# Kernel optimization log

Hardware: AMD Instinct MI355X
Metric: run time of the kernel (lower is better)

## Reference

```python
import jax, jax.numpy as jnp
import numpy as np

D = 1024   # hidden_size
H = 16     # n_head
K = 64     # head_size
B = 4
T = 1024
LAYER_ID = 12
NUM_LAYERS = 24
D_MIX = 32
D_DECAY = 64


def setup_inputs() -> dict:
    key = jax.random.key(0)
    ks = jax.random.split(key, 12)
    r01 = LAYER_ID / (NUM_LAYERS - 1)          # ratio_0_to_1
    r10 = 1.0 - LAYER_ID / NUM_LAYERS          # ratio_1_to_almost0
    ddd = jnp.arange(D, dtype=jnp.float32) / D
    maa = lambda p: (1.0 - ddd ** p).reshape(1, 1, D)
    inp = {}
    inp['x'] = jax.random.normal(ks[0], (B, T, D), jnp.float32)
    inp['time_maa_x'] = maa(r10)
    inp['time_maa_w'] = maa(r10)
    inp['time_maa_k'] = maa(r10)
    inp['time_maa_v'] = (1.0 - (ddd ** r10 + 0.3 * r01)).reshape(1, 1, D)
    inp['time_maa_r'] = maa(0.5 * r10)
    inp['time_maa_g'] = maa(0.5 * r10)
    # torch inits time_maa_w1 to zeros (trivial); use small uniform like w2 for a non-degenerate test
    inp['time_maa_w1'] = jax.random.uniform(ks[1], (D, D_MIX * 5), jnp.float32, -0.01, 0.01)
    inp['time_maa_w2'] = jax.random.uniform(ks[2], (5, D_MIX, D), jnp.float32, -0.01, 0.01)
    n = jnp.arange(D, dtype=jnp.float32)
    inp['time_decay'] = (-6.0 + 5.0 * (n / (D - 1)) ** (0.7 + 1.3 * r01)).reshape(1, 1, D)
    inp['time_decay_w1'] = jax.random.uniform(ks[3], (D, D_DECAY), jnp.float32, -0.01, 0.01)
    inp['time_decay_w2'] = jax.random.uniform(ks[4], (D_DECAY, D), jnp.float32, -0.01, 0.01)
    for nm, kk in zip(['W_r', 'W_k', 'W_v', 'W_g', 'W_o'], ks[5:10]):
        inp[nm] = jax.random.normal(kk, (D, D), jnp.float32) * 0.02
    inp['ln_w'] = jnp.ones((D,), jnp.float32)
    inp['ln_b'] = jnp.zeros((D,), jnp.float32)
    return inp


def _bidir_shift(x):
    # (x[i-1] + x[i+1]) / 2 with zero padding at the boundaries
    left = jnp.pad(x[:, :-1, :], ((0, 0), (1, 0), (0, 0)))
    right = jnp.pad(x[:, 1:, :], ((0, 0), (0, 1), (0, 0)))
    return 0.5 * (left + right)


def _lion_attention(r, k, v, w):
    # r,k,v,w: (B,H,T,Khd), w = -exp(decay) <= 0
    Tn = r.shape[2]
    cs = jnp.cumsum(w, axis=2)
    cs_b = cs - w
    shift_f = cs[:, :, Tn // 2:Tn // 2 + 1, :]
    shift_b = cs_b[:, :, Tn // 2:Tn // 2 + 1, :]
    cf = jnp.clip(cs - shift_f, -60.0, 60.0)
    cb = jnp.clip(cs_b - shift_b, -60.0, 60.0)
    # A_fwd = tril(Q*e^{cf} @ (K*e^{-cf})^T); A_bwd = triu(Q*e^{-cb} @ (K*e^{cb})^T, 1)
    A_f = jnp.einsum('bhik,bhjk->bhij', r * jnp.exp(cf), k * jnp.exp(-cf))
    A_b = jnp.einsum('bhik,bhjk->bhij', r * jnp.exp(-cb), k * jnp.exp(cb))
    idx = jnp.arange(Tn)
    lower = idx[:, None] >= idx[None, :]   # tril incl. diagonal
    A = jnp.where(lower, A_f, A_b)         # == tril(A_f) + triu(A_b, 1)
    return jnp.einsum('bhij,bhjk->bhik', A, v)


def reference(x, time_maa_x, time_maa_w, time_maa_k, time_maa_v, time_maa_r, time_maa_g,
              time_maa_w1, time_maa_w2, time_decay, time_decay_w1, time_decay_w2,
              W_r, W_k, W_v, W_g, W_o, ln_w, ln_b):
    Bn, Tn, Dn = x.shape
    Hh, Kk = H, Dn // H
    dxprev = _bidir_shift(x) - x
    # data-dependent token-shift mixing coefficients (LoRA-style)
    xxx = jnp.tanh((x + dxprev * time_maa_x) @ time_maa_w1)          # (B,T,5*32)
    mm = jnp.einsum('btfm,fmd->fbtd', xxx.reshape(Bn, Tn, 5, D_MIX), time_maa_w2)
    mw, mk, mv, mr, mg = mm[0], mm[1], mm[2], mm[3], mm[4]
    xw = x + dxprev * (time_maa_w + mw)
    xk = x + dxprev * (time_maa_k + mk)
    xv = x + dxprev * (time_maa_v + mv)
    xr = x + dxprev * (time_maa_r + mr)
    xg = x + dxprev * (time_maa_g + mg)
    r = xr @ W_r.T
    k = xk @ W_k.T
    v = xv @ W_v.T
    g = jax.nn.silu(xg @ W_g.T)
    w = time_decay + jnp.tanh(xw @ time_decay_w1) @ time_decay_w2   # (B,T,D)
    to_h = lambda t: t.reshape(Bn, Tn, Hh, Kk).transpose(0, 2, 1, 3)
    y = _lion_attention(to_h(r), to_h(k), to_h(v), -jnp.exp(to_h(w)))
    y = y.transpose(0, 2, 1, 3).reshape(Bn * Tn, Dn)
    # GroupNorm(n_head groups, eps = 1e-5 * head_size_divisor^2)
    eps = 1e-5 * 64.0
    yg = y.reshape(Bn * Tn, Hh, Kk)
    mu = jnp.mean(yg, axis=-1, keepdims=True)
    var = jnp.var(yg, axis=-1, keepdims=True)
    yn = ((yg - mu) * jax.lax.rsqrt(var + eps)).reshape(Bn * Tn, Dn) * ln_w + ln_b
    y = yn.reshape(Bn, Tn, Dn)
    return (y * g) @ W_o.T
```

## Files before the change

kernel.cpp:

```cpp
#include <hip/hip_runtime.h>
#include <math.h>

#define NB 4
#define TT 1024
#define DD 1024
#define NTOK 4096
#define ND (NTOK*DD)

typedef __attribute__((ext_vector_type(8))) short bh8;
typedef __attribute__((ext_vector_type(4))) float fx4;

__device__ __forceinline__ unsigned short f2bf(float f) {
    unsigned int b = __float_as_uint(f);
    b += 0x7fffu + ((b >> 16) & 1u);
    return (unsigned short)(b >> 16);
}

__device__ __forceinline__ unsigned pkbf(float a, float b) {
#if __has_builtin(__builtin_amdgcn_cvt_pk_bf16_f32)
    auto r = __builtin_amdgcn_cvt_pk_bf16_f32(a, b);
    unsigned u;
    __builtin_memcpy(&u, &r, 4);
    return u;
#else
// ... 21 lines not shown
    if (y < 5) {
        if (bx >= 512) return;
        const float* s = (y == 0) ? W_r : (y == 1) ? W_k : (y == 2) ? W_v : (y == 3) ? W_g : W_o;
        unsigned short* d = (y == 0) ? Wrb : (y == 1) ? Wkb : (y == 2) ? Wvb : (y == 3) ? Wgb : Wob;
        int i = (bx * 256 + tid) * 8;
        float4 a = *(const float4*)(s + i);
        float4 b = *(const float4*)(s + i + 4);
        uint4 o;
        o.x = pkbf(a.x, a.y);
        o.y = pkbf(a.z, a.w);
        o.z = pkbf(b.x, b.y);
        o.w = pkbf(b.z, b.w);
        *(uint4*)(d + i) = o;
    } else if (y == 5) {
        int o = bx * 256 + tid;
        int r = o & 1023, c = o >> 10;
        w1T[o] = f2bf(w1[r * 160 + c]);
    } else {
        if (bx < 256) {
            int o = bx * 256 + tid;
            int r = o & 1023, c = o >> 10;
            dw1T[o] = f2bf(dw1[r * 64 + c]);
        } else if (bx < 276) {
            int wi = bx - 256;
            int f = wi >> 2;
            int d = (wi & 3) * 256 + tid;
#pragma unroll 8
            for (int m = 0; m < 32; m++)
                w2T16[(size_t)(f * 1024 + d) * 32 + m] = f2bf(w2[(size_t)(f * 32 + m) * 1024 + d]);
        }
    }
}

__global__ __launch_bounds__(256) void k_mixx(const float* __restrict__ x,
                                              const float* __restrict__ maa_x,
                                              unsigned short* __restrict__ xmix16) {
    int base = (blockIdx.x * 256 + threadIdx.x) * 4;
    int t = (base >> 10) & 1023;
    int d = base & 1023;
    float4 xv = *(const float4*)(x + base);
    float4 xm = (t > 0)    ? *(const float4*)(x + base - 1024) : make_float4(0, 0, 0, 0);
    float4 xp = (t < 1023) ? *(const float4*)(x + base + 1024) : make_float4(0, 0, 0, 0);
    float4 ma = *(const float4*)(maa_x + d);
    uint2 o;
    float a0 = xv.x + (0.5f * (xm.x + xp.x) - xv.x) * ma.x;
    float a1 = xv.y + (0.5f * (xm.y + xp.y) - xv.y) * ma.y;
    float a2 = xv.z + (0.5f * (xm.z + xp.z) - xv.z) * ma.z;
    float a3 = xv.w + (0.5f * (xm.w + xp.w) - xv.w) * ma.w;
    o.x = pkbf(a0, a1);
    o.y = pkbf(a2, a3);
    *(uint2*)(xmix16 + base) = o;
}

__global__ __launch_bounds__(64) void k_xxx2(const unsigned short* __restrict__ xmix16,
                                             const unsigned short* __restrict__ w1T,
                                             unsigned short* __restrict__ xxx16) {
    int lane = threadIdx.x;
    int l15 = lane & 15, qd = lane >> 4;
    int m0 = blockIdx.x * 16;
    fx4 acc[10];
#pragma unroll
    for (int nt = 0; nt < 10; nt++)
#pragma unroll
        for (int r = 0; r < 4; r++) acc[nt][r] = 0.f;
#pragma unroll 2
    for (int kb = 0; kb < 1024; kb += 32) {
        bh8 af = *(const bh8*)(xmix16 + (size_t)(m0 + l15) * 1024 + kb + qd * 8);
#pragma unroll
        for (int nt = 0; nt < 10; nt++) {
            bh8 bf = *(const bh8*)(w1T + (size_t)(nt * 16 + l15) * 1024 + kb + qd * 8);
            acc[nt] = __builtin_amdgcn_mfma_f32_16x16x32_bf16(af, bf, acc[nt], 0, 0, 0);
        }
    }
#pragma unroll
    for (int nt = 0; nt < 10; nt++)
#pragma unroll
        for (int r = 0; r < 4; r++)
            xxx16[(size_t)(m0 + qd * 4 + r) * 160 + nt * 16 + l15] = f2bf(tanhf(acc[nt][r]));
}

__global__ __launch_bounds__(256, 2) void k_mmix(const float* __restrict__ x,
                                                 const unsigned short* __restrict__ xxx16,
                                                 const unsigned short* __restrict__ w2T16,
                                                 const float* __restrict__ maa_w,
                                                 const float* __restrict__ maa_k,
                                                 const float* __restrict__ maa_v,
                                                 const float* __restrict__ maa_r,
                                                 const float* __restrict__ maa_g,
                                                 unsigned short* __restrict__ xw16,
                                                 unsigned short* __restrict__ xk16,
                                                 unsigned short* __restrict__ xv16,
                                                 unsigned short* __restrict__ xr16,
                                                 unsigned short* __restrict__ xg16) {
    int tid = threadIdx.x;
    int w = tid >> 6, lane = tid & 63, l15 = lane & 15, qd = lane >> 4;
    int n0 = blockIdx.x * 64;
    int m0w = blockIdx.y * 128 + w * 32;
    const float* maap[5] = {maa_w, maa_k, maa_v, maa_r, maa_g};
    unsigned short* outp[5] = {xw16, xk16, xv16, xr16, xg16};
    float xin[8][4], dxv[8][4];
#pragma unroll
    for (int mi = 0; mi < 2; mi++)
#pragma unroll
        for (int r = 0; r < 4; r++) {
            int tok = m0w + mi * 16 + qd * 4 + r;
            int t = tok & 1023;
#pragma unroll
            for (int ni = 0; ni < 4; ni++) {
                int d = n0 + ni * 16 + l15;
                size_t idx = (size_t)tok * 1024 + d;
                float xv = x[idx];
                float xm1 = (t > 0)    ? x[idx - 1024] : 0.f;
                float xp1 = (t < 1023) ? x[idx + 1024] : 0.f;
                xin[mi * 4 + r][ni] = xv;
                dxv[mi * 4 + r][ni] = 0.5f * (xm1 + xp1) - xv;
            }
        }
#pragma unroll
    for (int f = 0; f < 5; f++) {
        bh8 af[2], bf[4];
#pragma unroll
        for (int mi = 0; mi < 2; mi++)
            af[mi] = *(const bh8*)(xxx16 + (size_t)(m0w + mi * 16 + l15) * 160 + f * 32 + qd * 8);
#pragma unroll
        for (int ni = 0; ni < 4; ni++)
            bf[ni] = *(const bh8*)(w2T16 + (size_t)(f * 1024 + n0 + ni * 16 + l15) * 32 + qd * 8);
        fx4 acc[2][4];
#pragma unroll
        for (int mi = 0; mi < 2; mi++)
#pragma unroll
            for (int ni = 0; ni < 4; ni++) {
#pragma unroll
                for (int r = 0; r < 4; r++) acc[mi][ni][r] = 0.f;
                acc[mi][ni] = __builtin_amdgcn_mfma_f32_16x16x32_bf16(af[mi], bf[ni], acc[mi][ni], 0, 0, 0);
            }
        const float* maa = maap[f];
        unsigned short* op = outp[f];
#pragma unroll
        for (int ni = 0; ni < 4; ni++) {
            float mv = maa[n0 + ni * 16 + l15];
#pragma unroll
            for (int mi = 0; mi < 2; mi++)
#pragma unroll
                for (int r = 0; r < 4; r++) {
                    float o = xin[mi * 4 + r][ni] + dxv[mi * 4 + r][ni] * (mv + acc[mi][ni][r]);
                    op[(size_t)(m0w + mi * 16 + qd * 4 + r) * 1024 + n0 + ni * 16 + l15] = f2bf(o);
                }
        }
    }
}

__global__ __launch_bounds__(64) void k_dec1m(const unsigned short* __restrict__ xw16,
                                              const unsigned short* __restrict__ dw1T,
                                              float* __restrict__ dech) {
    int lane = threadIdx.x;
    int l15 = lane & 15, qd = lane >> 4;
    int m0 = blockIdx.x * 16;
    fx4 acc[4];
#pragma unroll
    for (int nt = 0; nt < 4; nt++)
#pragma unroll
        for (int r = 0; r < 4; r++) acc[nt][r] = 0.f;
#pragma unroll 2
    for (int kb = 0; kb < 1024; kb += 32) {
        bh8 af = *(const bh8*)(xw16 + (size_t)(m0 + l15) * 1024 + kb + qd * 8);
#pragma unroll
        for (int nt = 0; nt < 4; nt++) {
            bh8 bf = *(const bh8*)(dw1T + (size_t)(nt * 16 + l15) * 1024 + kb + qd * 8);
            acc[nt] = __builtin_amdgcn_mfma_f32_16x16x32_bf16(af, bf, acc[nt], 0, 0, 0);
        }
    }
#pragma unroll
    for (int nt = 0; nt < 4; nt++)
#pragma unroll
        for (int r = 0; r < 4; r++)
            dech[(size_t)(m0 + qd * 4 + r) * 64 + nt * 16 + l15] = tanhf(acc[nt][r]);
}

__global__ __launch_bounds__(256) void k_dec2(const float* __restrict__ dech,
                                              const float* __restrict__ dw2,
                                              const float* __restrict__ tdec,
                                              float* __restrict__ ew) {
    __shared__ float hl[8][64];
    int tid = threadIdx.x;
    int tok0 = blockIdx.x * 8;
    {
        int l = tid;        hl[l >> 6][l & 63] = dech[tok0 * 64 + l];
        l = tid + 256;      hl[l >> 6][l & 63] = dech[tok0 * 64 + l];
    }
    __syncthreads();
#pragma unroll 1
    for (int c = 0; c < 4; c++) {
        int d = c * 256 + tid;
        float acc[8] = {};
#pragma unroll 8
        for (int j = 0; j < 64; j++) {
            float wv = dw2[j * 1024 + d];
#pragma unroll
            for (int g = 0; g < 8; g++) acc[g] = fmaf(hl[g][j], wv, acc[g]);
        }
        float td = tdec[d];
#pragma unroll
        for (int g = 0; g < 8; g++) ew[(tok0 + g) * 1024 + d] = -expf(td + acc[g]);
    }
}

__global__ __launch_bounds__(64) void k_scan1(const float* __restrict__ ew, float* __restrict__ segsum) {
    int bx = blockIdx.x;
    int b = bx >> 9, seg = (bx >> 4) & 31, dch = bx & 15;
    int d = dch * 64 + threadIdx.x;
    size_t base = ((size_t)(b * 1024 + seg * 32)) * 1024 + d;
    float s = 0.f;
#pragma unroll 8
    for (int t = 0; t < 32; t++) s += ew[base + (size_t)t * 1024];
    segsum[(b * 32 + seg) * 1024 + d] = s;
}

__global__ __launch_bounds__(64) void k_scan3(const float* __restrict__ ew, const float* __restrict__ segsum,
                                              float* __restrict__ cf, float* __restrict__ cb) {
    int bx = blockIdx.x;
    int b = bx >> 9, seg = (bx >> 4) & 31, dch = bx & 15;
    int d = dch * 64 + threadIdx.x;
    float run = 0.f, pre = 0.f, off16 = 0.f;
#pragma unroll
    for (int s = 0; s < 32; s++) {
        float tv = segsum[(b * 32 + s) * 1024 + d];
        if (s == seg) pre = run;
        if (s == 16) off16 = run;
        run += tv;
    }
    float e512 = ew[((size_t)(b * 1024 + 512)) * 1024 + d];
    float sb = off16;
    float sf = off16 + e512;
    float cum = pre;
    size_t base = ((size_t)(b * 1024 + seg * 32)) * 1024 + d;
#pragma unroll 4
    for (int t = 0; t < 32; t++) {
        float prev = cum;
        cum += ew[base + (size_t)t * 1024];
        cf[base + (size_t)t * 1024] = fminf(fmaxf(cum - sf, -60.f), 60.f);
        cb[base + (size_t)t * 1024] = fminf(fmaxf(prev - sb, -60.f), 60.f);
    }
}

__device__ __forceinline__ void gemm_body(const unsigned short* __restrict__ A,
                                          const unsigned short* __restrict__ W,
                                          int m0, int n0, int mode,
                                          float* __restrict__ Cf,
                                          unsigned short* __restrict__ O1,
                                          unsigned short* __restrict__ O2,
                                          const float* __restrict__ cfp,
                                          const float* __restrict__ cbp,
                                          char* smem) {
    int tid = threadIdx.x;
    int w = tid >> 6, lane = tid & 63, l15 = lane & 15, qd = lane >> 4;
    int wm = w >> 1, wn = w & 1;
    fx4 acc[4][4];
#pragma unroll
    for (int mt = 0; mt < 4; mt++)
#pragma unroll
        for (int nt = 0; nt < 4; nt++)
#pragma unroll
            for (int r = 0; r < 4; r++) acc[mt][nt][r] = 0.f;
    unsigned short* sA = (unsigned short*)smem;
    unsigned short* sB = (unsigned short*)(smem + 8192);
    int rowA = tid >> 2, cA = tid & 3;
    for (int kb = 0; kb < 1024; kb += 32) {
        __syncthreads();
        GLD16(A + (size_t)(m0 + rowA) * 1024 + kb + cA * 8,      sA + w * 512);
        GLD16(A + (size_t)(m0 + 64 + rowA) * 1024 + kb + cA * 8, sA + 2048 + w * 512);
        GLD16(W + (size_t)(n0 + rowA) * 1024 + kb + cA * 8,      sB + w * 512);
        GLD16(W + (size_t)(n0 + 64 + rowA) * 1024 + kb + cA * 8, sB + 2048 + w * 512);
        __syncthreads();
        bh8 af[4], bfr[4];
#pragma unroll
        for (int mt = 0; mt < 4; mt++)
            af[mt] = *(const bh8*)(sA + (wm * 64 + mt * 16 + l15) * 32 + qd * 8);
#pragma unroll
        for (int nt = 0; nt < 4; nt++)
            bfr[nt] = *(const bh8*)(sB + (wn * 64 + nt * 16 + l15) * 32 + qd * 8);
#pragma unroll
        for (int mt = 0; mt < 4; mt++)
#pragma unroll
            for (int nt = 0; nt < 4; nt++)
                acc[mt][nt] = __builtin_amdgcn_mfma_f32_16x16x32_bf16(af[mt], bfr[nt], acc[mt][nt], 0, 0, 0);
    }
    int mb = m0 + wm * 64, nb = n0 + wn * 64;
    if (mode <= 1) {
#pragma unroll
        for (int mt = 0; mt < 4; mt++)
#pragma unroll
            for (int nt = 0; nt < 4; nt++) {
                fx4 s = acc[mt][nt];
#pragma unroll
                for (int r = 0; r < 4; r++) {
                    float v = s[r];
                    if (mode == 1) v = v / (1.f + __expf(-v));
                    Cf[(size_t)(mb + mt * 16 + qd * 4 + r) * 1024 + nb + nt * 16 + l15] = v;
                }
            }
    } else if (mode <= 3) {
        float s1 = (mode == 2) ? 1.f : -1.f;
#pragma unroll
        for (int mt = 0; mt < 4; mt++)
#pragma unroll
            for (int nt = 0; nt < 4; nt++) {
                fx4 s = acc[mt][nt];
#pragma unroll
                for (int r = 0; r < 4; r++) {
                    size_t idx = (size_t)(mb + mt * 16 + qd * 4 + r) * 1024 + nb + nt * 16 + l15;
                    float v = s[r];
                    O1[idx] = f2bf(v * __expf(s1 * cfp[idx]));
                    O2[idx] = f2bf(v * __expf(-s1 * cbp[idx]));
                }
            }
    } else {
        __syncthreads();
        unsigned short* T = (unsigned short*)smem;
#pragma unroll
        for (int mt = 0; mt < 4; mt++)
#pragma unroll
            for (int nt = 0; nt < 4; nt++) {
                fx4 s = acc[mt][nt];
                int dl = wn * 64 + nt * 16 + l15;
                int tl = wm * 64 + mt * 16 + qd * 4;
                uint2 pk;
                pk.x = pkbf(s[0], s[1]);
                pk.y = pkbf(s[2], s[3]);
                *(uint2*)(T + dl * 136 + tl) = pk;
            }
        __syncthreads();
        int dl = tid >> 1, hf = tid & 1;
        int bq = m0 >> 10, t0 = m0 & 1023;
#pragma unroll
        for (int i = 0; i < 8; i++) {
            uint4 vv4 = *(const uint4*)(T + dl * 136 + hf * 64 + i * 8);
            *(uint4*)(O1 + (size_t)(bq * 1024 + n0 + dl) * 1024 + t0 + hf * 64 + i * 8) = vv4;
        }
    }
}


#define STA(dstbuf, g, kbv, Apt) GLD16(Apt + (size_t)(m0 + aBase + (g) * 32 + lr) * 1024 + (kbv) + swz, \
                                       (dstbuf) + (aBase + (g) * 32) * 64)
#define STB(dstbuf, s, kbv, Wpt) GLD16(Wpt + (size_t)(n0 + bBase + (s) * 64 + lr) * 1024 + (kbv) + swz, \
                                       (dstbuf) + (bBase + (s) * 64) * 64)

#define PHASE(mt0_, STAGE_, TAIL_) do {                                                  \
    bh8 aA0 = *(const bh8*)(sAc + arA + (mt0_) * 1024 + fc0);                            \
    bh8 aA1 = *(const bh8*)(sAc + arA + (mt0_) * 1024 + fc1);                            \
    bh8 aB0 = *(const bh8*)(sAc + arA + ((mt0_) + 1) * 1024 + fc0);                      \
    bh8 aB1 = *(const bh8*)(sAc + arA + ((mt0_) + 1) * 1024 + fc1);                      \
    STAGE_;                                                                              \
    BARF();                                                                              \
    asm volatile("s_waitcnt lgkmcnt(0)" ::: "memory");                                   \
    __builtin_amdgcn_s_setprio(1);                                                       \
    _Pragma("unroll")                                                                    \
    for (int nt = 0; nt < 4; ++nt) {                                                     \
        acc[(mt0_)][nt]     = __builtin_amdgcn_mfma_f32_16x16x32_bf16(aA0, bfr[nt][0], acc[(mt0_)][nt], 0, 0, 0);     \
        acc[(mt0_)][nt]     = __builtin_amdgcn_mfma_f32_16x16x32_bf16(aA1, bfr[nt][1], acc[(mt0_)][nt], 0, 0, 0);     \
        acc[(mt0_) + 1][nt] = __builtin_amdgcn_mfma_f32_16x16x32_bf16(aB0, bfr[nt][0], acc[(mt0_) + 1][nt], 0, 0, 0); \
        acc[(mt0_) + 1][nt] = __builtin_amdgcn_mfma_f32_16x16x32_bf16(aB1, bfr[nt][1], acc[(mt0_) + 1][nt], 0, 0, 0); \
    }                                                                                    \
    __builtin_amdgcn_s_setprio(0);                                                       \
    TAIL_;                                                                               \
    BARF();                                                                              \
} while (0)

__global__ __launch_bounds__(512, 2) void k_qkvg(const unsigned short* __restrict__ xr16,
                                                 const unsigned short* __restrict__ xk16,
                                                 const unsigned short* __restrict__ xv16,
                                                 const unsigned short* __restrict__ xg16,
                                                 const unsigned short* __restrict__ Wrb,
                                                 const unsigned short* __restrict__ Wkb,
                                                 const unsigned short* __restrict__ Wvb,
                                                 const unsigned short* __restrict__ Wgb,
                                                 unsigned short* __restrict__ qf, unsigned short* __restrict__ qb,
                                                 unsigned short* __restrict__ kf, unsigned short* __restrict__ kb,
                                                 unsigned short* __restrict__ vvt,
                                                 float* __restrict__ gg,
                                                 const float* __restrict__ cf, const float* __restrict__ cb) {
    __shared__ __align__(16) char smem[131072];
    unsigned short* sA0 = (unsigned short*)smem;
    unsigned short* sB0 = (unsigned short*)(smem + 32768);
    unsigned short* sA1 = (unsigned short*)(smem + 65536);
    unsigned short* sB1 = (unsigned short*)(smem + 98304);

    int flat = blockIdx.x;
    int wk = (flat & 7) * 32 + (flat >> 3);
    int gy = wk >> 6;
    int wi = wk & 63;
    int m0 = (wi >> 2) * 256, n0 = (wi & 3) * 256;

    const unsigned short* Ap = (gy == 0) ? xr16 : (gy == 1) ? xk16 : (gy == 2) ? xv16 : xg16;
// ... 66 lines not shown
#pragma unroll
                for (int r = 0; r < 4; r++) {
                    float v = acc[mt][nt][r];
                    v = v / (1.f + __expf(-v));
                    gg[(size_t)(mb + mt * 16 + qd * 4 + r) * 1024 + nb + nt * 16 + l15] = v;
                }
    } else if (gy == 2) {
        __syncthreads();
        unsigned short* T = (unsigned short*)smem;
        int bq = m0 >> 10, t0 = m0 & 1023;
#pragma unroll 1
        for (int h = 0; h < 2; ++h) {
            if (wm == h) {
#pragma unroll
                for (int mt = 0; mt < 8; mt++)
#pragma unroll
                    for (int nt = 0; nt < 4; nt++) {
                        int dl = wn * 64 + nt * 16 + l15;
                        int rl = mt * 16 + qd * 4;
                        uint2 pk;
                        pk.x = pkbf(acc[mt][nt][0], acc[mt][nt][1]);
                        pk.y = pkbf(acc[mt][nt][2], acc[mt][nt][3]);
                        *(uint2*)(T + dl * 136 + rl) = pk;
                    }
            }
            __syncthreads();
#pragma unroll
            for (int i = 0; i < 8; ++i) {
                int gch = i * 512 + tid;
                int d = gch >> 4, tch = gch & 15;
                uint4 vv = *(const uint4*)(T + d * 136 + tch * 8);
                *(uint4*)(vvt + (size_t)(bq * 1024 + n0 + d) * 1024 + t0 + h * 128 + tch * 8) = vv;
            }
            __syncthreads();
        }
    } else {
        unsigned short* O1 = gy ? kf : qf;
        unsigned short* O2 = gy ? kb : qb;
        float s1 = gy ? -1.f : 1.f;
#pragma unroll
        for (int mt = 0; mt < 8; mt++)
#pragma unroll
            for (int nt = 0; nt < 4; nt++)
#pragma unroll
                for (int r = 0; r < 4; r++) {
                    size_t idx = (size_t)(mb + mt * 16 + qd * 4 + r) * 1024 + nb + nt * 16 + l15;
                    float v = acc[mt][nt][r];
                    O1[idx] = f2bf(v * __expf(s1 * cf[idx]));
                    O2[idx] = f2bf(v * __expf(-s1 * cb[idx]));
                }
    }
}

__global__ __launch_bounds__(256, 2) void k_gemmo(const unsigned short* __restrict__ z16,
                                                  const unsigned short* __restrict__ Wob,
                                                  float* __restrict__ out) {
    __shared__ __align__(16) char smem[34816];
    gemm_body(z16, Wob, (blockIdx.x >> 3) * 128, (blockIdx.x & 7) * 128, 0, out,
              nullptr, nullptr, nullptr, nullptr, smem);
}

__global__ __launch_bounds__(256, 2) void k_attn(const unsigned short* __restrict__ qf,
                                                 const unsigned short* __restrict__ qb,
                                                 const unsigned short* __restrict__ kf,
                                                 const unsigned short* __restrict__ kb,
                                                 const unsigned short* __restrict__ vvt,
                                                 float* __restrict__ y) {
    __shared__ __align__(16) char smem[16384];
    unsigned short* sK = (unsigned short*)smem;
    unsigned short* sV = (unsigned short*)(smem + 8192);
    int tid = threadIdx.x;
    int w = tid >> 6, lane = tid & 63, l15 = lane & 15, qd = lane >> 4;
    int bid = blockIdx.x;
    int bh = (bid & 7) + ((bid >> 6) << 3);
    int ib = (bid >> 3) & 7;
    int b = bh >> 4, h = bh & 15;
    int i0w = ib * 128 + w * 32;
    int bt0 = b * 1024;
    const unsigned short* vrow = vvt + (size_t)(b * 1024 + h * 64 + w * 16 + l15) * 1024 + qd * 8;
    int fmax = (i0w + 31) >> 6;
    int bmin = i0w >> 6;
    int srcA = l15 + ((lane & 16) << 1);
    int srcB = srcA + 16;
    fx4 yacc[4][2];
#pragma unroll
    for (int mt = 0; mt < 4; mt++)
#pragma unroll
        for (int nt = 0; nt < 2; nt++)
#pragma unroll
            for (int r = 0; r < 4; r++) yacc[mt][nt][r] = 0.f;

    for (int phase = 0; phase < 2; phase++) {
        const unsigned short* Q = phase ? qb : qf;
        const unsigned short* K = phase ? kb : kf;
        bh8 qfr[2][2];
#pragma unroll
        for (int nt = 0; nt < 2; nt++)
#pragma unroll
            for (int ks = 0; ks < 2; ks++)
                qfr[nt][ks] = *(const bh8*)(Q + (size_t)(bt0 + i0w + nt * 16 + l15) * 1024
                                              + h * 64 + ks * 32 + qd * 8);
        int jlo = phase == 0 ? 0 : 2 * ib;
        int jhi = phase == 0 ? 2 * ib + 1 : 15;
        const unsigned short* krow = K + (size_t)(bt0 + w * 16 + l15) * 1024 + h * 64 + qd * 8;
        for (int jt = jlo; jt <= jhi; jt++) {
            int jb = jt * 64;
            __syncthreads();
            GLD16(krow + (size_t)jb * 1024,        sK + w * 512);
            GLD16(krow + (size_t)jb * 1024 + 32,   sK + 2048 + w * 512);
            GLD16(vrow + jb,                        sV + w * 512);
            GLD16(vrow + jb + 32,                   sV + 2048 + w * 512);
            __syncthreads();
            bool active = (phase == 0) ? (jt <= fmax) : (jt >= bmin);
            if (!active) continue;
            bool needmask = (phase == 0) ? (jb + 63 > i0w) : (i0w + 31 >= jb);
            bh8 kc[8];
#pragma unroll
            for (int fi = 0; fi < 8; fi++)
                kc[fi] = *(const bh8*)(sK + fi * 512 + lane * 8);
            fx4 sacc[4][2];
#pragma unroll
            for (int mt = 0; mt < 4; mt++)
#pragma unroll
                for (int nt = 0; nt < 2; nt++)
#pragma unroll
                    for (int r = 0; r < 4; r++) sacc[mt][nt][r] = 0.f;
#pragma unroll
            for (int ks = 0; ks < 2; ks++)
#pragma unroll
                for (int mt = 0; mt < 4; mt++)
#pragma unroll
                    for (int nt = 0; nt < 2; nt++)
                        sacc[mt][nt] = __builtin_amdgcn_mfma_f32_16x16x32_bf16(kc[ks * 4 + mt], qfr[nt][ks], sacc[mt][nt], 0, 0, 0);
            uint2 pk[4][2];
#pragma unroll
            for (int mt = 0; mt < 4; mt++)
#pragma unroll
                for (int nt = 0; nt < 2; nt++) {
                    fx4 s = sacc[mt][nt];
                    if (needmask) {
                        int ii = i0w + nt * 16 + l15;
                        int jj0 = jb + mt * 16 + qd * 4;
#pragma unroll
                        for (int r = 0; r < 4; r++) {
                            bool keep = (phase == 0) ? (ii >= jj0 + r) : (ii < jj0 + r);
                            if (!keep) s[r] = 0.f;
                        }
                    }
                    pk[mt][nt].x = pkbf(s[0], s[1]);
                    pk[mt][nt].y = pkbf(s[2], s[3]);
                }
            bh8 vc[8];
#pragma unroll
            for (int fi = 0; fi < 8; fi++)
                vc[fi] = *(const bh8*)(sV + fi * 512 + lane * 8);
#pragma unroll
            for (int ks2 = 0; ks2 < 2; ks2++) {
#pragma unroll
                for (int nt = 0; nt < 2; nt++) {
                    int lox  = __shfl((int)pk[2 * ks2][nt].x,     srcA);
                    int hix  = __shfl((int)pk[2 * ks2 + 1][nt].x, srcA);
                    int loy  = __shfl((int)pk[2 * ks2][nt].y,     srcA);
                    int hiy  = __shfl((int)pk[2 * ks2 + 1][nt].y, srcA);
                    int lox2 = __shfl((int)pk[2 * ks2][nt].x,     srcB);
                    int hix2 = __shfl((int)pk[2 * ks2 + 1][nt].x, srcB);
                    int loy2 = __shfl((int)pk[2 * ks2][nt].y,     srcB);
                    int hiy2 = __shfl((int)pk[2 * ks2 + 1][nt].y, srcB);
                    union { int4 i; bh8 h; } cv;
                    cv.i.x = (qd & 2) ? hix  : lox;
                    cv.i.y = (qd & 2) ? hiy  : loy;
                    cv.i.z = (qd & 2) ? hix2 : lox2;
                    cv.i.w = (qd & 2) ? hiy2 : loy2;
#pragma unroll
                    for (int mt = 0; mt < 4; mt++)
                        yacc[mt][nt] = __builtin_amdgcn_mfma_f32_16x16x32_bf16(vc[ks2 * 4 + mt], cv.h, yacc[mt][nt], 0, 0, 0);
                }
            }
        }
    }
#pragma unroll
    for (int mt = 0; mt < 4; mt++)
#pragma unroll
        for (int nt = 0; nt < 2; nt++) {
            fx4 s = yacc[mt][nt];
            float4 o; o.x = s[0]; o.y = s[1]; o.z = s[2]; o.w = s[3];
            *(float4*)&y[(size_t)(bt0 + i0w + nt * 16 + l15) * 1024 + h * 64 + mt * 16 + qd * 4] = o;
        }
}

__global__ __launch_bounds__(256) void k_gn(const float* __restrict__ y,
                                            const float* __restrict__ g,
                                            const float* __restrict__ lnw,
                                            const float* __restrict__ lnb,
                                            unsigned short* __restrict__ z16) {
    int tid = threadIdx.x;
    int lane = tid & 63;
    int wv = tid >> 6;
    int group = blockIdx.x * 4 + wv;
    int tok = group >> 4, h = group & 15;
    int d = h * 64 + lane;
    size_t idx = (size_t)tok * 1024 + d;
    float val = y[idx];
    float s = val, s2 = val * val;
#pragma unroll
    for (int off = 32; off > 0; off >>= 1) {
        s  += __shfl_xor(s, off, 64);
        s2 += __shfl_xor(s2, off, 64);
    }
    float mu = s * (1.f / 64.f);
    float var = s2 * (1.f / 64.f) - mu * mu;
    float inv = rsqrtf(var + 6.4e-4f);
    float yn = (val - mu) * inv * lnw[d] + lnb[d];
    z16[idx] = f2bf(yn * g[idx]);
}

extern "C" void kernel_launch(void* const* d_in, const int* in_sizes, int n_in,
                              void* d_out, int out_size, void* d_ws, size_t ws_size,
                              hipStream_t stream) {
    const float* x     = (const float*)d_in[0];
    const float* maa_x = (const float*)d_in[1];
    const float* maa_w = (const float*)d_in[2];
    const float* maa_k = (const float*)d_in[3];
    const float* maa_v = (const float*)d_in[4];
    const float* maa_r = (const float*)d_in[5];
    const float* maa_g = (const float*)d_in[6];
    const float* w1    = (const float*)d_in[7];
    const float* w2    = (const float*)d_in[8];
    const float* tdec  = (const float*)d_in[9];
    const float* dw1   = (const float*)d_in[10];
    const float* dw2   = (const float*)d_in[11];
    const float* W_r   = (const float*)d_in[12];
    const float* W_k   = (const float*)d_in[13];
    const float* W_v   = (const float*)d_in[14];
    const float* W_g   = (const float*)d_in[15];
    const float* W_o   = (const float*)d_in[16];
    const float* lnw   = (const float*)d_in[17];
    const float* lnb   = (const float*)d_in[18];

    float* ws = (float*)d_ws;
    size_t o = 0;
    float* dech   = ws + o; o += 262144;
    float* segsum = ws + o; o += 131072;
    float* ew     = ws + o; o += 4194304;
    float* cf     = ws + o; o += 4194304;
    float* cb     = ws + o; o += 4194304;
    float* gg     = ws + o; o += 4194304;
    unsigned short* us = (unsigned short*)(ws + o);
    size_t u = 0;
    unsigned short* xmix16 = us + u; u += 4194304;
    unsigned short* xw16 = us + u; u += 4194304;
    unsigned short* xr16 = us + u; u += 4194304;
    unsigned short* xk16 = us + u; u += 4194304;
    unsigned short* xv16 = us + u; u += 4194304;
    unsigned short* xg16 = us + u; u += 4194304;
    unsigned short* qf   = us + u; u += 4194304;
    unsigned short* qb   = us + u; u += 4194304;
    unsigned short* kf   = us + u; u += 4194304;
    unsigned short* kb   = us + u; u += 4194304;
    unsigned short* vvt  = us + u; u += 4194304;
    unsigned short* Wrb  = us + u; u += 1048576;
    unsigned short* Wkb  = us + u; u += 1048576;
    unsigned short* Wvb  = us + u; u += 1048576;
    unsigned short* Wgb  = us + u; u += 1048576;
    unsigned short* Wob  = us + u; u += 1048576;
    unsigned short* w1T  = us + u; u += 163840;
    unsigned short* dw1T = us + u; u += 65536;
    unsigned short* xxx16 = us + u; u += 655360;
    unsigned short* w2T16 = us + u; u += 163840;
    float* yb0 = cf;
    unsigned short* z16 = xr16;

    k_prep<<<dim3(640, 7), 256, 0, stream>>>(W_r, W_k, W_v, W_g, W_o, w1, dw1, w2,
                                             Wrb, Wkb, Wvb, Wgb, Wob, w1T, dw1T, w2T16);
    k_mixx<<<4096, 256, 0, stream>>>(x, maa_x, xmix16);
    k_xxx2<<<256, 64, 0, stream>>>(xmix16, w1T, xxx16);
    k_mmix<<<dim3(16, 32), 256, 0, stream>>>(x, xxx16, w2T16, maa_w, maa_k, maa_v, maa_r, maa_g,
                                             xw16, xk16, xv16, xr16, xg16);
    k_dec1m<<<256, 64, 0, stream>>>(xw16, dw1T, dech);
    k_dec2<<<512, 256, 0, stream>>>(dech, dw2, tdec, ew);
    k_scan1<<<2048, 64, 0, stream>>>(ew, segsum);
    k_scan3<<<2048, 64, 0, stream>>>(ew, segsum, cf, cb);
    k_qkvg<<<dim3(256), dim3(512), 0, stream>>>(xr16, xk16, xv16, xg16, Wrb, Wkb, Wvb, Wgb,
                                                qf, qb, kf, kb, vvt, gg, cf, cb);
    k_attn<<<512, 256, 0, stream>>>(qf, qb, kf, kb, vvt, yb0);
    k_gn<<<16384, 256, 0, stream>>>(yb0, gg, lnw, lnb, z16);
    k_gemmo<<<256, 256, 0, stream>>>(z16, Wob, (float*)d_out);
}
```

Before: 343.7 us.

## Split-K small GEMMs, triple-buffer output GEMM, double-tile attention loads, cooperative launch

The two skinny LoRA GEMMs (xxx and decay-w1) now split K across four waves per block and reduce the partials through shared memory, giving each block more parallelism. The output projection moves to a new triple-buffered GEMM with swizzled LDS, explicit vmcnt waits, setprio around the MFMAs and a remapped block order. The attention kernel loads two K/V tiles per barrier pair, which halves the synchronisations but doubles its LDS use. The QKVG GEMM is now started with hipLaunchCooperativeKernel, which may add launch overhead and adds no clear speed benefit.

```diff
diff --git a/kernel.cpp b/kernel.cpp
--- a/kernel.cpp
+++ b/kernel.cpp
@@ -97,10 +97,12 @@
     *(uint2*)(xmix16 + base) = o;
 }
 
-__global__ __launch_bounds__(64) void k_xxx2(const unsigned short* __restrict__ xmix16,
-                                             const unsigned short* __restrict__ w1T,
-                                             unsigned short* __restrict__ xxx16) {
-    int lane = threadIdx.x;
+__global__ __launch_bounds__(256) void k_xxx2(const unsigned short* __restrict__ xmix16,
+                                              const unsigned short* __restrict__ w1T,
+                                              unsigned short* __restrict__ xxx16) {
+    __shared__ __align__(16) float red[4][10][64][4];
+    int tid = threadIdx.x;
+    int lane = tid & 63, wv = tid >> 6;
     int l15 = lane & 15, qd = lane >> 4;
     int m0 = blockIdx.x * 16;
     fx4 acc[10];
@@ -108,8 +110,9 @@
     for (int nt = 0; nt < 10; nt++)
 #pragma unroll
         for (int r = 0; r < 4; r++) acc[nt][r] = 0.f;
+    int kb0 = wv * 256;
 #pragma unroll 2
-    for (int kb = 0; kb < 1024; kb += 32) {
+    for (int kb = kb0; kb < kb0 + 256; kb += 32) {
         bh8 af = *(const bh8*)(xmix16 + (size_t)(m0 + l15) * 1024 + kb + qd * 8);
 #pragma unroll
         for (int nt = 0; nt < 10; nt++) {
@@ -119,9 +122,20 @@
     }
 #pragma unroll
     for (int nt = 0; nt < 10; nt++)
-#pragma unroll
-        for (int r = 0; r < 4; r++)
-            xxx16[(size_t)(m0 + qd * 4 + r) * 160 + nt * 16 + l15] = f2bf(tanhf(acc[nt][r]));
+        *(fx4*)&red[wv][nt][lane][0] = acc[nt];
+    __syncthreads();
+    if (wv == 0) {
+#pragma unroll
+        for (int nt = 0; nt < 10; nt++) {
+            fx4 s = *(const fx4*)&red[0][nt][lane][0];
+            s = s + *(const fx4*)&red[1][nt][lane][0];
+            s = s + *(const fx4*)&red[2][nt][lane][0];
+            s = s + *(const fx4*)&red[3][nt][lane][0];
+#pragma unroll
+            for (int r = 0; r < 4; r++)
+                xxx16[(size_t)(m0 + qd * 4 + r) * 160 + nt * 16 + l15] = f2bf(tanhf(s[r]));
+        }
+    }
 }
 
 __global__ __launch_bounds__(256, 2) void k_mmix(const float* __restrict__ x,
@@ -195,10 +209,12 @@
     }
 }
 
-__global__ __launch_bounds__(64) void k_dec1m(const unsigned short* __restrict__ xw16,
-                                              const unsigned short* __restrict__ dw1T,
-                                              float* __restrict__ dech) {
-    int lane = threadIdx.x;
+__global__ __launch_bounds__(256) void k_dec1m(const unsigned short* __restrict__ xw16,
+                                               const unsigned short* __restrict__ dw1T,
+                                               float* __restrict__ dech) {
+    __shared__ __align__(16) float red[4][4][64][4];
+    int tid = threadIdx.x;
+    int lane = tid & 63, wv = tid >> 6;
     int l15 = lane & 15, qd = lane >> 4;
     int m0 = blockIdx.x * 16;
     fx4 acc[4];
@@ -206,8 +222,9 @@
     for (int nt = 0; nt < 4; nt++)
 #pragma unroll
         for (int r = 0; r < 4; r++) acc[nt][r] = 0.f;
+    int kb0 = wv * 256;
 #pragma unroll 2
-    for (int kb = 0; kb < 1024; kb += 32) {
+    for (int kb = kb0; kb < kb0 + 256; kb += 32) {
         bh8 af = *(const bh8*)(xw16 + (size_t)(m0 + l15) * 1024 + kb + qd * 8);
 #pragma unroll
         for (int nt = 0; nt < 4; nt++) {
@@ -217,9 +234,20 @@
     }
 #pragma unroll
     for (int nt = 0; nt < 4; nt++)
-#pragma unroll
-        for (int r = 0; r < 4; r++)
-            dech[(size_t)(m0 + qd * 4 + r) * 64 + nt * 16 + l15] = tanhf(acc[nt][r]);
+        *(fx4*)&red[wv][nt][lane][0] = acc[nt];
+    __syncthreads();
+    if (wv == 0) {
+#pragma unroll
+        for (int nt = 0; nt < 4; nt++) {
+            fx4 s = *(const fx4*)&red[0][nt][lane][0];
+            s = s + *(const fx4*)&red[1][nt][lane][0];
+            s = s + *(const fx4*)&red[2][nt][lane][0];
+            s = s + *(const fx4*)&red[3][nt][lane][0];
+#pragma unroll
+            for (int r = 0; r < 4; r++)
+                dech[(size_t)(m0 + qd * 4 + r) * 64 + nt * 16 + l15] = tanhf(s[r]);
+        }
+    }
 }
 
 __global__ __launch_bounds__(256) void k_dec2(const float* __restrict__ dech,
@@ -287,104 +315,6 @@
         cb[base + (size_t)t * 1024] = fminf(fmaxf(prev - sb, -60.f), 60.f);
     }
 }
-
-__device__ __forceinline__ void gemm_body(const unsigned short* __restrict__ A,
-                                          const unsigned short* __restrict__ W,
-                                          int m0, int n0, int mode,
-                                          float* __restrict__ Cf,
-                                          unsigned short* __restrict__ O1,
-                                          unsigned short* __restrict__ O2,
-                                          const float* __restrict__ cfp,
-                                          const float* __restrict__ cbp,
-                                          char* smem) {
-    int tid = threadIdx.x;
-    int w = tid >> 6, lane = tid & 63, l15 = lane & 15, qd = lane >> 4;
-    int wm = w >> 1, wn = w & 1;
-    fx4 acc[4][4];
-#pragma unroll
-    for (int mt = 0; mt < 4; mt++)
-#pragma unroll
-        for (int nt = 0; nt < 4; nt++)
-#pragma unroll
-            for (int r = 0; r < 4; r++) acc[mt][nt][r] = 0.f;
-    unsigned short* sA = (unsigned short*)smem;
-    unsigned short* sB = (unsigned short*)(smem + 8192);
-    int rowA = tid >> 2, cA = tid & 3;
-    for (int kb = 0; kb < 1024; kb += 32) {
-        __syncthreads();
-        GLD16(A + (size_t)(m0 + rowA) * 1024 + kb + cA * 8,      sA + w * 512);
-        GLD16(A + (size_t)(m0 + 64 + rowA) * 1024 + kb + cA * 8, sA + 2048 + w * 512);
-        GLD16(W + (size_t)(n0 + rowA) * 1024 + kb + cA * 8,      sB + w * 512);
-        GLD16(W + (size_t)(n0 + 64 + rowA) * 1024 + kb + cA * 8, sB + 2048 + w * 512);
-        __syncthreads();
-        bh8 af[4], bfr[4];
-#pragma unroll
-        for (int mt = 0; mt < 4; mt++)
-            af[mt] = *(const bh8*)(sA + (wm * 64 + mt * 16 + l15) * 32 + qd * 8);
-#pragma unroll
-        for (int nt = 0; nt < 4; nt++)
-            bfr[nt] = *(const bh8*)(sB + (wn * 64 + nt * 16 + l15) * 32 + qd * 8);
-#pragma unroll
-        for (int mt = 0; mt < 4; mt++)
-#pragma unroll
-            for (int nt = 0; nt < 4; nt++)
-                acc[mt][nt] = __builtin_amdgcn_mfma_f32_16x16x32_bf16(af[mt], bfr[nt], acc[mt][nt], 0, 0, 0);
-    }
-    int mb = m0 + wm * 64, nb = n0 + wn * 64;
-    if (mode <= 1) {
-#pragma unroll
-        for (int mt = 0; mt < 4; mt++)
-#pragma unroll
-            for (int nt = 0; nt < 4; nt++) {
-                fx4 s = acc[mt][nt];
-#pragma unroll
-                for (int r = 0; r < 4; r++) {
-                    float v = s[r];
-                    if (mode == 1) v = v / (1.f + __expf(-v));
-                    Cf[(size_t)(mb + mt * 16 + qd * 4 + r) * 1024 + nb + nt * 16 + l15] = v;
-                }
-            }
-    } else if (mode <= 3) {
-        float s1 = (mode == 2) ? 1.f : -1.f;
-#pragma unroll
-        for (int mt = 0; mt < 4; mt++)
-#pragma unroll
-            for (int nt = 0; nt < 4; nt++) {
-                fx4 s = acc[mt][nt];
-#pragma unroll
-                for (int r = 0; r < 4; r++) {
-                    size_t idx = (size_t)(mb + mt * 16 + qd * 4 + r) * 1024 + nb + nt * 16 + l15;
-                    float v = s[r];
-                    O1[idx] = f2bf(v * __expf(s1 * cfp[idx]));
-                    O2[idx] = f2bf(v * __expf(-s1 * cbp[idx]));
-                }
-            }
-    } else {
-        __syncthreads();
-        unsigned short* T = (unsigned short*)smem;
-#pragma unroll
-        for (int mt = 0; mt < 4; mt++)
-#pragma unroll
-            for (int nt = 0; nt < 4; nt++) {
-                fx4 s = acc[mt][nt];
-                int dl = wn * 64 + nt * 16 + l15;
-                int tl = wm * 64 + mt * 16 + qd * 4;
-                uint2 pk;
-                pk.x = pkbf(s[0], s[1]);
-                pk.y = pkbf(s[2], s[3]);
-                *(uint2*)(T + dl * 136 + tl) = pk;
-            }
-        __syncthreads();
-        int dl = tid >> 1, hf = tid & 1;
-        int bq = m0 >> 10, t0 = m0 & 1023;
-#pragma unroll
-        for (int i = 0; i < 8; i++) {
-            uint4 vv4 = *(const uint4*)(T + dl * 136 + hf * 64 + i * 8);
-            *(uint4*)(O1 + (size_t)(bq * 1024 + n0 + dl) * 1024 + t0 + hf * 64 + i * 8) = vv4;
-        }
-    }
-}
-
 
 #define STA(dstbuf, g, kbv, Apt) GLD16(Apt + (size_t)(m0 + aBase + (g) * 32 + lr) * 1024 + (kbv) + swz, \
                                        (dstbuf) + (aBase + (g) * 32) * 64)
@@ -557,12 +487,149 @@
     }
 }
 
-__global__ __launch_bounds__(256, 2) void k_gemmo(const unsigned short* __restrict__ z16,
+template<int NW, int BNv>
+__device__ __forceinline__ void gemm_v5(const unsigned short* __restrict__ A,
+                                        const unsigned short* __restrict__ W,
+                                        int m0, int n0, int mode,
+                                        float* __restrict__ Cf,
+                                        unsigned short* __restrict__ O1,
+                                        unsigned short* __restrict__ O2,
+                                        const float* __restrict__ cfp,
+                                        const float* __restrict__ cbp,
+                                        char* smem) {
+    constexpr int AR = 128 / NW;
+    constexpr int AG = AR / 16;
+    constexpr int BR = BNv / NW;
+    constexpr int BG = BR / 16;
+    constexpr int LPW = AG + BG;
+    constexpr int SLOT = (128 + BNv) * 64;
+    constexpr int WNC = BNv / 64;
+
+    int tid = threadIdx.x;
+    int lane = tid & 63, w = tid >> 6;
+    int l15 = lane & 15, qd = lane >> 4;
+    int wm = w / WNC, wn = w % WNC;
+    int lr = lane >> 2, lb = lane & 3;
+    int gblk = lb ^ ((lr >> 1) & 3);
+    const unsigned short* aSrc = A + (size_t)(m0 + w * AR + lr) * 1024 + gblk * 8;
+    const unsigned short* bSrc = W + (size_t)(n0 + w * BR + lr) * 1024 + gblk * 8;
+    int rc = (qd ^ ((l15 >> 1) & 3)) * 8;
+    int arow = (wm * 64 + l15) * 32 + rc;
+    int brow = (wn * 64 + l15) * 32 + rc;
+
+    auto stage = [&](int off, int kbv) {
+        unsigned short* _sa = (unsigned short*)(smem + off);
+        unsigned short* _sb = _sa + 128 * 32;
+#pragma unroll
+        for (int i = 0; i < AG; ++i)
+            GLD16(aSrc + kbv + (size_t)i * 16 * 1024, _sa + (w * AR + i * 16) * 32);
+#pragma unroll
+        for (int i = 0; i < BG; ++i)
+            GLD16(bSrc + kbv + (size_t)i * 16 * 1024, _sb + (w * BR + i * 16) * 32);
+    };
+
+    fx4 acc[4][4];
+#pragma unroll
+    for (int mt = 0; mt < 4; mt++)
+#pragma unroll
+        for (int nt = 0; nt < 4; nt++)
+#pragma unroll
+            for (int r = 0; r < 4; r++) acc[mt][nt][r] = 0.f;
+
+    stage(0, 0);
+    stage(SLOT, 32);
+    if constexpr (LPW == 3) asm volatile("s_waitcnt vmcnt(3)" ::: "memory");
+    else                    asm volatile("s_waitcnt vmcnt(4)" ::: "memory");
+    BARF();
+
+    int oc = 0, on = SLOT, o2 = 2 * SLOT;
+#pragma unroll 1
+    for (int t = 0; t < 32; ++t) {
+        if (t < 30) stage(o2, (t + 2) * 32);
+        const unsigned short* cA = (const unsigned short*)(smem + oc);
+        const unsigned short* cB = cA + 128 * 32;
+        bh8 a[4], b[4];
+#pragma unroll
+        for (int mt = 0; mt < 4; ++mt) a[mt] = *(const bh8*)(cA + arow + mt * 512);
+#pragma unroll
+        for (int nt = 0; nt < 4; ++nt) b[nt] = *(const bh8*)(cB + brow + nt * 512);
+        __builtin_amdgcn_s_setprio(1);
+#pragma unroll
+        for (int nt = 0; nt < 4; ++nt)
+#pragma unroll
+            for (int mt = 0; mt < 4; ++mt)
+                acc[mt][nt] = __builtin_amdgcn_mfma_f32_16x16x32_bf16(a[mt], b[nt], acc[mt][nt], 0, 0, 0);
+        __builtin_amdgcn_s_setprio(0);
+        asm volatile("s_waitcnt lgkmcnt(0)" ::: "memory");
+        if (t < 30) {
+            if constexpr (LPW == 3) asm volatile("s_waitcnt vmcnt(3)" ::: "memory");
+            else                    asm volatile("s_waitcnt vmcnt(4)" ::: "memory");
+        } else if (t == 30) {
+            asm volatile("s_waitcnt vmcnt(0)" ::: "memory");
+        }
+        BARF();
+        int tmp = oc; oc = on; on = o2; o2 = tmp;
+    }
+
+    int mb = m0 + wm * 64, nb = n0 + wn * 64;
+    if (mode <= 1) {
+#pragma unroll
+        for (int mt = 0; mt < 4; mt++)
+#pragma unroll
+            for (int nt = 0; nt < 4; nt++)
+#pragma unroll
+                for (int r = 0; r < 4; r++) {
+                    float v = acc[mt][nt][r];
+                    if (mode == 1) v = v / (1.f + __expf(-v));
+                    Cf[(size_t)(mb + mt * 16 + qd * 4 + r) * 1024 + nb + nt * 16 + l15] = v;
+                }
+    } else if (mode <= 3) {
+        float s1 = (mode == 2) ? 1.f : -1.f;
+#pragma unroll
+        for (int mt = 0; mt < 4; mt++)
+#pragma unroll
+            for (int nt = 0; nt < 4; nt++)
+#pragma unroll
+                for (int r = 0; r < 4; r++) {
+                    size_t idx = (size_t)(mb + mt * 16 + qd * 4 + r) * 1024 + nb + nt * 16 + l15;
+                    float v = acc[mt][nt][r];
+                    O1[idx] = f2bf(v * __expf(s1 * cfp[idx]));
+                    O2[idx] = f2bf(v * __expf(-s1 * cbp[idx]));
+                }
+    } else {
+        unsigned short* T = (unsigned short*)smem;
+        int bq = m0 >> 10, t0 = m0 & 1023;
+#pragma unroll
+        for (int mt = 0; mt < 4; mt++)
+#pragma unroll
+            for (int nt = 0; nt < 4; nt++) {
+                int dl = wn * 64 + nt * 16 + l15;
+                int tl = wm * 64 + mt * 16 + qd * 4;
+                uint2 pk2;
+                pk2.x = pkbf(acc[mt][nt][0], acc[mt][nt][1]);
+                pk2.y = pkbf(acc[mt][nt][2], acc[mt][nt][3]);
+                *(uint2*)(T + dl * 136 + tl) = pk2;
+            }
+        asm volatile("s_waitcnt lgkmcnt(0)" ::: "memory");
+        BARF();
+#pragma unroll
+        for (int p = 0; p < 8; ++p) {
+            int idx = p * (NW * 64) + tid;
+            int dd = idx >> 4, u = idx & 15;
+            uint4 vv = *(const uint4*)(T + dd * 136 + u * 8);
+            *(uint4*)(O1 + (size_t)(bq * 1024 + n0 + dd) * 1024 + t0 + u * 8) = vv;
+        }
+    }
+}
+
+__global__ __launch_bounds__(256, 3) void k_gemmo(const unsigned short* __restrict__ z16,
                                                   const unsigned short* __restrict__ Wob,
                                                   float* __restrict__ out) {
-    __shared__ __align__(16) char smem[34816];
-    gemm_body(z16, Wob, (blockIdx.x >> 3) * 128, (blockIdx.x & 7) * 128, 0, out,
-              nullptr, nullptr, nullptr, nullptr, smem);
+    __shared__ __align__(16) char smem[49152];
+    int flat = blockIdx.x;
+    int wkid = (flat & 7) * 32 + (flat >> 3);
+    int m0 = (wkid >> 3) * 128, n0 = (wkid & 7) * 128;
+    gemm_v5<4, 128>(z16, Wob, m0, n0, 0, out, nullptr, nullptr, nullptr, nullptr, smem);
 }
 
 __global__ __launch_bounds__(256, 2) void k_attn(const unsigned short* __restrict__ qf,
@@ -571,9 +638,9 @@
                                                  const unsigned short* __restrict__ kb,
                                                  const unsigned short* __restrict__ vvt,
                                                  float* __restrict__ y) {
-    __shared__ __align__(16) char smem[16384];
+    __shared__ __align__(16) char smem[32768];
     unsigned short* sK = (unsigned short*)smem;
-    unsigned short* sV = (unsigned short*)(smem + 8192);
+    unsigned short* sV = (unsigned short*)(smem + 16384);
     int tid = threadIdx.x;
     int w = tid >> 6, lane = tid & 63, l15 = lane & 15, qd = lane >> 4;
     int bid = blockIdx.x;
@@ -608,77 +675,87 @@
         int jlo = phase == 0 ? 0 : 2 * ib;
         int jhi = phase == 0 ? 2 * ib + 1 : 15;
         const unsigned short* krow = K + (size_t)(bt0 + w * 16 + l15) * 1024 + h * 64 + qd * 8;
-        for (int jt = jlo; jt <= jhi; jt++) {
-            int jb = jt * 64;
+        for (int jt2 = jlo; jt2 <= jhi; jt2 += 2) {
             __syncthreads();
-            GLD16(krow + (size_t)jb * 1024,        sK + w * 512);
-            GLD16(krow + (size_t)jb * 1024 + 32,   sK + 2048 + w * 512);
-            GLD16(vrow + jb,                        sV + w * 512);
-            GLD16(vrow + jb + 32,                   sV + 2048 + w * 512);
+#pragma unroll
+            for (int u = 0; u < 2; ++u) {
+                size_t jb = (size_t)(jt2 + u) * 64;
+                GLD16(krow + jb * 1024,        sK + u * 4096 + w * 512);
+                GLD16(krow + jb * 1024 + 32,   sK + u * 4096 + 2048 + w * 512);
+                GLD16(vrow + jb,               sV + u * 4096 + w * 512);
+                GLD16(vrow + jb + 32,          sV + u * 4096 + 2048 + w * 512);
+            }
             __syncthreads();
-            bool active = (phase == 0) ? (jt <= fmax) : (jt >= bmin);
-            if (!active) continue;
-            bool needmask = (phase == 0) ? (jb + 63 > i0w) : (i0w + 31 >= jb);
-            bh8 kc[8];
-#pragma unroll
-            for (int fi = 0; fi < 8; fi++)
-                kc[fi] = *(const bh8*)(sK + fi * 512 + lane * 8);
-            fx4 sacc[4][2];
-#pragma unroll
-            for (int mt = 0; mt < 4; mt++)
-#pragma unroll
-                for (int nt = 0; nt < 2; nt++)
-#pragma unroll
-                    for (int r = 0; r < 4; r++) sacc[mt][nt][r] = 0.f;
-#pragma unroll
-            for (int ks = 0; ks < 2; ks++)
+#pragma unroll
+            for (int u = 0; u < 2; ++u) {
+                int jt = jt2 + u;
+                int jb = jt * 64;
+                const unsigned short* bK = sK + u * 4096;
+                const unsigned short* bV = sV + u * 4096;
+                bool active = (phase == 0) ? (jt <= fmax) : (jt >= bmin);
+                if (!active) continue;
+                bool needmask = (phase == 0) ? (jb + 63 > i0w) : (i0w + 31 >= jb);
+                bh8 kc[8];
+#pragma unroll
+                for (int fi = 0; fi < 8; fi++)
+                    kc[fi] = *(const bh8*)(bK + fi * 512 + lane * 8);
+                fx4 sacc[4][2];
 #pragma unroll
                 for (int mt = 0; mt < 4; mt++)
 #pragma unroll
                     for (int nt = 0; nt < 2; nt++)
-                        sacc[mt][nt] = __builtin_amdgcn_mfma_f32_16x16x32_bf16(kc[ks * 4 + mt], qfr[nt][ks], sacc[mt][nt], 0, 0, 0);
-            uint2 pk[4][2];
-#pragma unroll
-            for (int mt = 0; mt < 4; mt++)
-#pragma unroll
-                for (int nt = 0; nt < 2; nt++) {
-                    fx4 s = sacc[mt][nt];
-                    if (needmask) {
-                        int ii = i0w + nt * 16 + l15;
-                        int jj0 = jb + mt * 16 + qd * 4;
-#pragma unroll
-                        for (int r = 0; r < 4; r++) {
-                            bool keep = (phase == 0) ? (ii >= jj0 + r) : (ii < jj0 + r);
-                            if (!keep) s[r] = 0.f;
+#pragma unroll
+                        for (int r = 0; r < 4; r++) sacc[mt][nt][r] = 0.f;
+#pragma unroll
+                for (int ks = 0; ks < 2; ks++)
+#pragma unroll
+                    for (int mt = 0; mt < 4; mt++)
+#pragma unroll
+                        for (int nt = 0; nt < 2; nt++)
+                            sacc[mt][nt] = __builtin_amdgcn_mfma_f32_16x16x32_bf16(kc[ks * 4 + mt], qfr[nt][ks], sacc[mt][nt], 0, 0, 0);
+                uint2 pk[4][2];
+#pragma unroll
+                for (int mt = 0; mt < 4; mt++)
+#pragma unroll
+                    for (int nt = 0; nt < 2; nt++) {
+                        fx4 s = sacc[mt][nt];
+                        if (needmask) {
+                            int ii = i0w + nt * 16 + l15;
+                            int jj0 = jb + mt * 16 + qd * 4;
+#pragma unroll
+                            for (int r = 0; r < 4; r++) {
+                                bool keep = (phase == 0) ? (ii >= jj0 + r) : (ii < jj0 + r);
+                                if (!keep) s[r] = 0.f;
+                            }
                         }
+                        pk[mt][nt].x = pkbf(s[0], s[1]);
+                        pk[mt][nt].y = pkbf(s[2], s[3]);
                     }
-                    pk[mt][nt].x = pkbf(s[0], s[1]);
-                    pk[mt][nt].y = pkbf(s[2], s[3]);
-                }
-            bh8 vc[8];
-#pragma unroll
-            for (int fi = 0; fi < 8; fi++)
-                vc[fi] = *(const bh8*)(sV + fi * 512 + lane * 8);
-#pragma unroll
-            for (int ks2 = 0; ks2 < 2; ks2++) {
-#pragma unroll
-                for (int nt = 0; nt < 2; nt++) {
-                    int lox  = __shfl((int)pk[2 * ks2][nt].x,     srcA);
-                    int hix  = __shfl((int)pk[2 * ks2 + 1][nt].x, srcA);
-                    int loy  = __shfl((int)pk[2 * ks2][nt].y,     srcA);
-                    int hiy  = __shfl((int)pk[2 * ks2 + 1][nt].y, srcA);
-                    int lox2 = __shfl((int)pk[2 * ks2][nt].x,     srcB);
-                    int hix2 = __shfl((int)pk[2 * ks2 + 1][nt].x, srcB);
-                    int loy2 = __shfl((int)pk[2 * ks2][nt].y,     srcB);
-                    int hiy2 = __shfl((int)pk[2 * ks2 + 1][nt].y, srcB);
-                    union { int4 i; bh8 h; } cv;
-                    cv.i.x = (qd & 2) ? hix  : lox;
-                    cv.i.y = (qd & 2) ? hiy  : loy;
-                    cv.i.z = (qd & 2) ? hix2 : lox2;
-                    cv.i.w = (qd & 2) ? hiy2 : loy2;
-#pragma unroll
-                    for (int mt = 0; mt < 4; mt++)
-                        yacc[mt][nt] = __builtin_amdgcn_mfma_f32_16x16x32_bf16(vc[ks2 * 4 + mt], cv.h, yacc[mt][nt], 0, 0, 0);
+                bh8 vc[8];
+#pragma unroll
+                for (int fi = 0; fi < 8; fi++)
+                    vc[fi] = *(const bh8*)(bV + fi * 512 + lane * 8);
+#pragma unroll
+                for (int ks2 = 0; ks2 < 2; ks2++) {
+#pragma unroll
+                    for (int nt = 0; nt < 2; nt++) {
+                        int lox  = __shfl((int)pk[2 * ks2][nt].x,     srcA);
+                        int hix  = __shfl((int)pk[2 * ks2 + 1][nt].x, srcA);
+                        int loy  = __shfl((int)pk[2 * ks2][nt].y,     srcA);
+                        int hiy  = __shfl((int)pk[2 * ks2 + 1][nt].y, srcA);
+                        int lox2 = __shfl((int)pk[2 * ks2][nt].x,     srcB);
+                        int hix2 = __shfl((int)pk[2 * ks2 + 1][nt].x, srcB);
+                        int loy2 = __shfl((int)pk[2 * ks2][nt].y,     srcB);
+                        int hiy2 = __shfl((int)pk[2 * ks2 + 1][nt].y, srcB);
+                        union { int4 i; bh8 h; } cv;
+                        cv.i.x = (qd & 2) ? hix  : lox;
+                        cv.i.y = (qd & 2) ? hiy  : loy;
+                        cv.i.z = (qd & 2) ? hix2 : lox2;
+                        cv.i.w = (qd & 2) ? hiy2 : loy2;
+#pragma unroll
+                        for (int mt = 0; mt < 4; mt++)
+                            yacc[mt][nt] = __builtin_amdgcn_mfma_f32_16x16x32_bf16(vc[ks2 * 4 + mt], cv.h, yacc[mt][nt], 0, 0, 0);
+                    }
                 }
             }
         }
@@ -778,15 +855,21 @@
     k_prep<<<dim3(640, 7), 256, 0, stream>>>(W_r, W_k, W_v, W_g, W_o, w1, dw1, w2,
                                              Wrb, Wkb, Wvb, Wgb, Wob, w1T, dw1T, w2T16);
     k_mixx<<<4096, 256, 0, stream>>>(x, maa_x, xmix16);
-    k_xxx2<<<256, 64, 0, stream>>>(xmix16, w1T, xxx16);
+    k_xxx2<<<256, 256, 0, stream>>>(xmix16, w1T, xxx16);
     k_mmix<<<dim3(16, 32), 256, 0, stream>>>(x, xxx16, w2T16, maa_w, maa_k, maa_v, maa_r, maa_g,
                                              xw16, xk16, xv16, xr16, xg16);
-    k_dec1m<<<256, 64, 0, stream>>>(xw16, dw1T, dech);
+    k_dec1m<<<256, 256, 0, stream>>>(xw16, dw1T, dech);
     k_dec2<<<512, 256, 0, stream>>>(dech, dw2, tdec, ew);
     k_scan1<<<2048, 64, 0, stream>>>(ew, segsum);
     k_scan3<<<2048, 64, 0, stream>>>(ew, segsum, cf, cb);
-    k_qkvg<<<dim3(256), dim3(512), 0, stream>>>(xr16, xk16, xv16, xg16, Wrb, Wkb, Wvb, Wgb,
-                                                qf, qb, kf, kb, vvt, gg, cf, cb);
+    {
+        void* ka[16];
+        ka[0]  = (void*)&xr16; ka[1]  = (void*)&xk16; ka[2]  = (void*)&xv16; ka[3]  = (void*)&xg16;
+        ka[4]  = (void*)&Wrb;  ka[5]  = (void*)&Wkb;  ka[6]  = (void*)&Wvb;  ka[7]  = (void*)&Wgb;
+        ka[8]  = (void*)&qf;   ka[9]  = (void*)&qb;   ka[10] = (void*)&kf;   ka[11] = (void*)&kb;
+        ka[12] = (void*)&vvt;  ka[13] = (void*)&gg;   ka[14] = (void*)&cf;   ka[15] = (void*)&cb;
+        hipLaunchCooperativeKernel((const void*)k_qkvg, dim3(256), dim3(512), ka, 0, stream);
+    }
     k_attn<<<512, 256, 0, stream>>>(qf, qb, kf, kb, vvt, yb0);
     k_gn<<<16384, 256, 0, stream>>>(yb0, gg, lnw, lnb, z16);
     k_gemmo<<<256, 256, 0, stream>>>(z16, Wob, (float*)d_out);
```

Result: slower. 377.7 us (+9.9%).
